# Performance work log

Hardware: AMD Instinct MI355X
Metric: run time of the kernel (lower is better)

The kernel has to match this reference:

```python
import jax, jax.numpy as jnp
import numpy as np
from jax.scipy.special import erfc
from jax.scipy.linalg import solve_triangular

B, N, M = 1024, 256, 320


def _conv(x, w, b, s):
    # torch Conv2d(k=5, stride=s, padding=2)
    y = jax.lax.conv_general_dilated(x, w, (s, s), ((2, 2), (2, 2)),
                                     dimension_numbers=('NCHW', 'OIHW', 'NCHW'))
    return y + b[None, :, None, None]


def _deconv(x, w, b, s):
    # torch ConvTranspose2d(k=5, stride=s, padding=2, output_padding=s-1); w is [Cin,Cout,5,5]
    w2 = jnp.flip(w, (2, 3)).transpose(1, 0, 2, 3)
    pad = (2, 2 + (s - 1))
    y = jax.lax.conv_general_dilated(x, w2, (1, 1), (pad, pad), lhs_dilation=(s, s),
                                     dimension_numbers=('NCHW', 'OIHW', 'NCHW'))
    return y + b[None, :, None, None]


def _gdn(x, beta, gamma, inverse):
    # divisive normalization: norm = 1x1 conv of x^2 with gamma, plus beta
    norm = jnp.einsum('oc,bchw->bohw', gamma, x * x) + beta[None, :, None, None]
    return x * jnp.sqrt(norm) if inverse else x * jax.lax.rsqrt(norm)


def _forward(x, noise, w1, b1, beta1, gamma1, w2, b2, beta2, gamma2, w3, b3,
             dw1, db1, ibeta1, igamma1, dw2, db2, ibeta2, igamma2, dw3, db3,
             mean, scale, H):
    # analysis transform g_a
    a = _gdn(_conv(x, w1, b1, 2), beta1, gamma1, False)   # [B,N,16,16]
    a = _gdn(_conv(a, w2, b2, 2), beta2, gamma2, False)   # [B,N,8,8]
    y = _conv(a, w3, b3, 1)                               # [B,M,8,8]
    Bs, C, h, w = y.shape
    yf = y.reshape(Bs, C, h * w)                          # [B,M,64]
    mask = jnp.tril(jnp.ones((64, 64), jnp.float32), -1)  # strictly lower
    H_tril = H * mask                                     # [M,64,64]
    # w_res = (I - H_tril) y, per channel
    w_res = yf - jnp.einsum('cij,bcj->bci', H_tril, yf)
    # GaussianConditional training-mode quantize: additive uniform noise
    w_res_hat = w_res + noise.reshape(Bs, C, h * w)
    # likelihoods under N(mean, scale) with scale lower bound 0.11
    s = jnp.maximum(scale, 0.11)[None]                    # [1,M,8,8]
    v = jnp.abs(w_res_hat.reshape(Bs, C, h, w) - mean[None])
    c = -(2 ** -0.5)
    upper = 0.5 * erfc(c * ((0.5 - v) / s))
    lower = 0.5 * erfc(c * ((-0.5 - v) / s))
    lik = jnp.maximum(upper - lower, 1e-9)
    # y_hat = (I - H_tril)^{-1} w_res_hat via unit-lower triangular solve
    A = jnp.eye(64, dtype=jnp.float32)[None] - H_tril     # [M,64,64]
    y_hat = solve_triangular(A, w_res_hat.transpose(1, 2, 0), lower=True,
                             unit_diagonal=True).transpose(2, 0, 1).reshape(Bs, C, h, w)
    # synthesis transform g_s
    d = _gdn(_deconv(y_hat, dw1, db1, 1), ibeta1, igamma1, True)
    d = _gdn(_deconv(d, dw2, db2, 2), ibeta2, igamma2, True)
    x_hat = jnp.clip(_deconv(d, dw3, db3, 2), 0.0, 1.0)
    return x_hat, lik


def setup_inputs() -> dict:
    key = jax.random.key(0)
    ks = jax.random.split(key, 16)
    rn = lambda k, sh: 0.02 * jax.random.normal(k, sh, dtype=jnp.float32)
    eye_g = 0.1 * jnp.eye(N, dtype=jnp.float32) + 1e-3
    return {
        'x': jax.random.uniform(ks[0], (B, 2, 32, 32), dtype=jnp.float32),
        'noise': jax.random.uniform(ks[1], (B, M, 8, 8), dtype=jnp.float32) - 0.5,
        'w1': rn(ks[2], (N, 2, 5, 5)), 'b1': jnp.zeros((N,), jnp.float32),
        'beta1': jnp.ones((N,), jnp.float32), 'gamma1': eye_g,
        'w2': rn(ks[3], (N, N, 5, 5)), 'b2': jnp.zeros((N,), jnp.float32),
        'beta2': jnp.ones((N,), jnp.float32), 'gamma2': eye_g,
        'w3': rn(ks[4], (M, N, 5, 5)), 'b3': jnp.zeros((M,), jnp.float32),
        'dw1': rn(ks[5], (M, N, 5, 5)), 'db1': jnp.zeros((N,), jnp.float32),
        'ibeta1': jnp.ones((N,), jnp.float32), 'igamma1': eye_g,
        'dw2': rn(ks[6], (N, N, 5, 5)), 'db2': jnp.zeros((N,), jnp.float32),
        'ibeta2': jnp.ones((N,), jnp.float32), 'igamma2': eye_g,
        'dw3': rn(ks[7], (N, 2, 5, 5)), 'db3': jnp.zeros((2,), jnp.float32),
        'mean': jnp.zeros((M, 8, 8), jnp.float32),
        'scale': jnp.ones((M, 8, 8), jnp.float32),
        'H': rn(ks[8], (M, 64, 64)),
    }


def reference(x, noise, w1, b1, beta1, gamma1, w2, b2, beta2, gamma2, w3, b3,
              dw1, db1, ibeta1, igamma1, dw2, db2, ibeta2, igamma2, dw3, db3,
              mean, scale, H):
    return _forward(x, noise, w1, b1, beta1, gamma1, w2, b2, beta2, gamma2, w3, b3,
                    dw1, db1, ibeta1, igamma1, dw2, db2, ibeta2, igamma2, dw3, db3,
                    mean, scale, H)
```

## Files before the change

### kernel.cpp

```cpp
#include <hip/hip_runtime.h>
#include <math.h>

typedef unsigned short u16;
typedef unsigned long long u64t;
typedef __bf16 bf16x8 __attribute__((ext_vector_type(8)));
typedef float f32x4 __attribute__((ext_vector_type(4)));
struct alignas(8) u16x4 { u16 x0, x1, x2, x3; };

__device__ __forceinline__ int ufl(int v) { return __builtin_amdgcn_readfirstlane(v); }
__device__ __forceinline__ u16 f2b(float f) {
    unsigned u = __float_as_uint(f);
    return (u16)((u + 0x7FFFu + ((u >> 16) & 1u)) >> 16);
}
__device__ __forceinline__ float b2f(u16 h) { return __uint_as_float(((unsigned)h) << 16); }
__device__ __forceinline__ u16 tob(float v) { return f2b(v); }
__device__ __forceinline__ u16 tob(u16 v)   { return v; }


template<int CIN, int COUT>
__global__ __launch_bounds__(256) void rk_fwd(const float* __restrict__ w, u16* __restrict__ a) {
    int j = (blockIdx.x * 256 + threadIdx.x) * 2;
    if (j >= 25 * COUT * CIN) return;
    int ci = j % CIN; int r = j / CIN; int co = r % COUT; int t = r / COUT;
    u16 lo = f2b(w[(co * CIN + ci) * 25 + t]);
    u16 hi = f2b(w[(co * CIN + ci + 1) * 25 + t]);
    *(unsigned*)&a[j] = (unsigned)lo | ((unsigned)hi << 16);
}
__global__ __launch_bounds__(256) void rk_d1(const float* __restrict__ w, u16* __restrict__ a) {
    int j = (blockIdx.x * 256 + threadIdx.x) * 2;
    if (j >= 25 * 256 * 320) return;
    int ci = j % 320; int r = j / 320; int co = r % 256; int tp = r / 256;
    int ky = 4 - tp / 5, kx = 4 - tp % 5;
    u16 lo = f2b(w[(ci * 256 + co) * 25 + ky * 5 + kx]);
    u16 hi = f2b(w[((ci + 1) * 256 + co) * 25 + ky * 5 + kx]);
    *(unsigned*)&a[j] = (unsigned)lo | ((unsigned)hi << 16);
}
__global__ __launch_bounds__(256) void rk_d2(const float* __restrict__ w, u16* __restrict__ a) {
    int j = (blockIdx.x * 256 + threadIdx.x) * 2;
    if (j >= 36 * 256 * 256) return;
    int ci = j % 256; int r = j / 256; int co = r % 256; int qt = r / 256;
    int q = qt / 9, tt = qt % 9;
    int qy = q >> 1, qx = q & 1, ty = tt / 3, tx = tt % 3;
    u16 lo = 0, hi = 0;
    if (ty < 3 - qy && tx < 3 - qx) {
        int widx = (qy + 2 * ty) * 5 + (qx + 2 * tx);
        lo = f2b(w[(ci * 256 + co) * 25 + widx]);
        hi = f2b(w[((ci + 1) * 256 + co) * 25 + widx]);
    }
    *(unsigned*)&a[j] = (unsigned)lo | ((unsigned)hi << 16);
}
__global__ __launch_bounds__(256) void rk_d3(const float* __restrict__ w, float* __restrict__ a) {
    int i = blockIdx.x * 256 + threadIdx.x;
    if (i >= 4 * 256 * 2 * 16) return;
    int t = i % 16; int r = i / 16; int co = r % 2; int r2 = r / 2; int ci = r2 % 256; int q = r2 / 256;
    int qy = q >> 1, qx = q & 1;
    float v = 0.f;
    if (t < 9) {
        int ty = t / 3, tx = t % 3;
        if (ty < 3 - qy && tx < 3 - qx) v = w[(ci * 2 + co) * 25 + (qy + 2 * ty) * 5 + (qx + 2 * tx)];
    }
    a[i] = v;
}
__global__ __launch_bounds__(256) void rk_g(const float* __restrict__ g, u16* __restrict__ a) {
    int j = (blockIdx.x * 256 + threadIdx.x) * 2;
    if (j >= 256 * 256) return;
    u16 lo = f2b(g[j]);
    u16 hi = f2b(g[j + 1]);
    *(unsigned*)&a[j] = (unsigned)lo | ((unsigned)hi << 16);
}

template<int CIN, int COUT, int S, int MT, typename TIN, typename TOUT>
__global__ __launch_bounds__(256)
void mconv(const TIN* __restrict__ in, const u16* __restrict__ A,
           const float* __restrict__ bias, TOUT* __restrict__ out)
{
    constexpr bool O16 = (sizeof(TOUT) == 2);
    constexpr int HIN = 8 * S, HP = 7 * S + 5, CHUNK = 64, STRIDE = CHUNK + 8;
    constexpr int NCH = CIN / CHUNK;
    constexpr int SP = HP * HP;
    constexpr int BSE = SP * STRIDE;
    constexpr int OSE = O16 ? COUT * 64 : 0;
    constexpr int NIT = 50;
    __shared__ u16 bs[(BSE > OSE) ? BSE : OSE];

    const int b = blockIdx.x;
    const int tid = threadIdx.x;
    const int lane = tid & 63, wv = tid >> 6;
    const int lm = lane & 15, quad = lane >> 4;
    const int cob = wv * (MT * 16);
    const TIN* inb = in + (size_t)b * CIN * (HIN * HIN);

    int bofs[4];
#pragma unroll
    for (int nt = 0; nt < 4; ++nt) {
        int px = nt * 16 + lm, oy = px >> 3, ox = px & 7;
        bofs[nt] = (S * oy * HP + S * ox) * STRIDE + quad * 8;
    }

    f32x4 acc[MT][4];
#pragma unroll
    for (int m = 0; m < MT; ++m)
#pragma unroll
        for (int n = 0; n < 4; ++n) acc[m][n] = (f32x4){0.f, 0.f, 0.f, 0.f};

#pragma unroll 1
    for (int ch = 0; ch < NCH; ++ch) {
        if (ch) __syncthreads();
        unsigned* bz = (unsigned*)bs;
        for (int i = tid; i < BSE / 2; i += 256) bz[i] = 0u;
        __syncthreads();
        for (int i = tid; i < (CHUNK / 4) * (HIN * HIN); i += 256) {
            int px = i % (HIN * HIN), cg = i / (HIN * HIN);
            int iy = px / HIN, ix = px % HIN;
            const TIN* ip = inb + (size_t)(ch * CHUNK + cg * 4) * (HIN * HIN) + px;
            u16x4 p;
            p.x0 = tob(ip[0]);
            p.x1 = tob(ip[HIN * HIN]);
            p.x2 = tob(ip[2 * HIN * HIN]);
            p.x3 = tob(ip[3 * HIN * HIN]);
            *(u16x4*)&bs[((iy + 2) * HP + ix + 2) * STRIDE + cg * 4] = p;
        }
        __syncthreads();

        const u16* Ar[MT];
#pragma unroll
        for (int m = 0; m < MT; ++m)
            Ar[m] = A + ch * CHUNK + quad * 8 + (size_t)(cob + m * 16 + lm) * CIN;

        bf16x8 af0[MT], af1[MT];
#pragma unroll
        for (int m = 0; m < MT; ++m) af0[m] = *(const bf16x8*)(Ar[m]);

#pragma unroll 1
        for (int it = 0; it < NIT; it += 2) {
            const int tapB = (it + 1) >> 1, kcB = (it + 1) & 1;
            const size_t oB = (size_t)tapB * (COUT * CIN) + kcB * 32;
#pragma unroll
            for (int m = 0; m < MT; ++m) af1[m] = *(const bf16x8*)(Ar[m] + oB);
            {
                const int tap = it >> 1, kc = it & 1;
                const int tofs = ((tap / 5) * HP + (tap % 5)) * STRIDE + kc * 32;
                bf16x8 bf[4];
#pragma unroll
                for (int nt = 0; nt < 4; ++nt)
                    bf[nt] = *(const bf16x8*)&bs[bofs[nt] + tofs];
#pragma unroll
                for (int m = 0; m < MT; ++m)
#pragma unroll
                    for (int nt = 0; nt < 4; ++nt)
                        acc[m][nt] = __builtin_amdgcn_mfma_f32_16x16x32_bf16(af0[m], bf[nt], acc[m][nt], 0, 0, 0);
            }
            if (it + 2 < NIT) {
                const size_t oC = (size_t)((it + 2) >> 1) * (COUT * CIN);
#pragma unroll
                for (int m = 0; m < MT; ++m) af0[m] = *(const bf16x8*)(Ar[m] + oC);
            }
            {
                const int tofs = ((tapB / 5) * HP + (tapB % 5)) * STRIDE + kcB * 32;
                bf16x8 bf[4];
#pragma unroll
                for (int nt = 0; nt < 4; ++nt)
                    bf[nt] = *(const bf16x8*)&bs[bofs[nt] + tofs];
#pragma unroll
                for (int m = 0; m < MT; ++m)
#pragma unroll
                    for (int nt = 0; nt < 4; ++nt)
                        acc[m][nt] = __builtin_amdgcn_mfma_f32_16x16x32_bf16(af1[m], bf[nt], acc[m][nt], 0, 0, 0);
            }
        }
    }

    if constexpr (O16) {
        __syncthreads();
#pragma unroll
        for (int m = 0; m < MT; ++m)
#pragma unroll
            for (int nt = 0; nt < 4; ++nt)
#pragma unroll
                for (int r = 0; r < 4; ++r) {
                    int co = cob + m * 16 + quad * 4 + r;
                    bs[co * 64 + nt * 16 + lm] = f2b(acc[m][nt][r] + bias[co]);
                }
        __syncthreads();
        u16* ob = out + (size_t)b * COUT * 64;
        const unsigned* osw = (const unsigned*)bs;
#pragma unroll
        for (int it = 0; it < COUT / 16; ++it) {
            int v = it * 256 + tid;
            unsigned lo = osw[v * 2], hi = osw[v * 2 + 1];
            *(u64t*)&ob[v * 4] = (u64t)lo | ((u64t)hi << 32);
        }
    } else {
        float* ob = (float*)out + (size_t)b * COUT * 64;
#pragma unroll
        for (int m = 0; m < MT; ++m)
#pragma unroll
            for (int nt = 0; nt < 4; ++nt) {
                int px = nt * 16 + lm;
#pragma unroll
                for (int r = 0; r < 4; ++r) {
                    int co = cob + m * 16 + quad * 4 + r;
                    ob[(size_t)co * 64 + px] = acc[m][nt][r] + bias[co];
                }
            }
    }
}

template<bool INVERSE, int IMG, int YOFF, int RS>
__global__ __launch_bounds__(256)
void gdnm(u16* __restrict__ x, const float* __restrict__ beta,
          const u16* __restrict__ Ag)
{
    constexpr int STR = 264;
    __shared__ u16 xb[256 * 64];
    __shared__ u16 xq[64 * STR];
    const int tid = threadIdx.x;
    const int lane = tid & 63, wv = tid >> 6;
    const int lm = lane & 15, quad = lane >> 4;
    const int cob = wv * 64;
    u16* xg = x + (size_t)blockIdx.x * IMG + (size_t)blockIdx.y * YOFF;

#pragma unroll
    for (int it = 0; it < 16; ++it) {
        int v = it * 256 + tid;
        int ch = v >> 4, pxg = (v & 15) * 4;
        *(u64t*)&xb[v * 4] = *(const u64t*)&xg[(size_t)ch * RS + pxg];
    }
    __syncthreads();

    {
        const int px = tid & 63, g = tid >> 6;
#pragma unroll
        for (int w = 0; w < 32; ++w) {
            int ci = g * 64 + ((w + px) & 31) * 2;
            float x0 = b2f(xb[ci * 64 + px]);
            float x1 = b2f(xb[(ci + 1) * 64 + px]);
            unsigned pk = (unsigned)f2b(x0 * x0) | ((unsigned)f2b(x1 * x1) << 16);
            *(unsigned*)&xq[px * STR + ci] = pk;
        }
    }
    __syncthreads();

    f32x4 acc[4][4];
#pragma unroll
    for (int m = 0; m < 4; ++m)
#pragma unroll
        for (int n = 0; n < 4; ++n) acc[m][n] = (f32x4){0.f, 0.f, 0.f, 0.f};

#pragma unroll 1
    for (int kc = 0; kc < 8; ++kc) {
        bf16x8 bf[4];
#pragma unroll
        for (int nt = 0; nt < 4; ++nt)
            bf[nt] = *(const bf16x8*)&xq[(nt * 16 + lm) * STR + kc * 32 + quad * 8];
        bf16x8 af[4];
#pragma unroll
        for (int m = 0; m < 4; ++m)
            af[m] = *(const bf16x8*)(Ag + (size_t)(cob + m * 16 + lm) * 256 + kc * 32 + quad * 8);
#pragma unroll
        for (int m = 0; m < 4; ++m)
#pragma unroll
            for (int nt = 0; nt < 4; ++nt)
                acc[m][nt] = __builtin_amdgcn_mfma_f32_16x16x32_bf16(af[m], bf[nt], acc[m][nt], 0, 0, 0);
    }

#pragma unroll
    for (int m = 0; m < 4; ++m)
#pragma unroll
        for (int nt = 0; nt < 4; ++nt)
#pragma unroll
            for (int r = 0; r < 4; ++r) {
                int co = cob + m * 16 + quad * 4 + r;
                int px = nt * 16 + lm;
                float norm = acc[m][nt][r] + beta[co];
                float rr = INVERSE ? sqrtf(norm) : rsqrtf(norm);
                u16* p = &xb[co * 64 + px];
                *p = f2b(b2f(*p) * rr);
            }
    __syncthreads();

#pragma unroll
    for (int it = 0; it < 16; ++it) {
        int v = it * 256 + tid;
        int ch = v >> 4, pxg = (v & 15) * 4;
        *(u64t*)&xg[(size_t)ch * RS + pxg] = *(const u64t*)&xb[v * 4];
    }
}

__global__ __launch_bounds__(256)
void mdeconv2(const u16* __restrict__ in, const u16* __restrict__ A2,
              const float* __restrict__ bias, u16* __restrict__ out)
{
    constexpr int STRIDE = 264;
    __shared__ u16 bs[100 * STRIDE];
    __shared__ u16 os[256 * 64];
    const int b = blockIdx.x, tid = threadIdx.x;
    const int lane = tid & 63, wv = tid >> 6, lm = lane & 15, quad = lane >> 4;
    const int cob = wv * 64;
    const u16* inb = in + (size_t)b * 256 * 64;

    unsigned* bz = (unsigned*)bs;
    for (int i = tid; i < 100 * STRIDE / 2; i += 256) bz[i] = 0u;
    __syncthreads();
    for (int i = tid; i < 64 * 64; i += 256) {
        int px = i & 63, cg = i >> 6;
        int iy = px >> 3, ix = px & 7;
        const u16* ip = inb + (size_t)cg * 4 * 64 + px;
        u16x4 p;
        p.x0 = ip[0]; p.x1 = ip[64]; p.x2 = ip[128]; p.x3 = ip[192];
        *(u16x4*)&bs[((iy + 1) * 10 + ix + 1) * STRIDE + cg * 4] = p;
    }
    __syncthreads();

    int bofs[4];
#pragma unroll
    for (int nt = 0; nt < 4; ++nt) {
        int sp = nt * 16 + lm, sy = sp >> 3, sx = sp & 7;
        bofs[nt] = ((sy + 2) * 10 + sx + 2) * STRIDE + quad * 8;
    }

#pragma unroll
    for (int qy = 0; qy < 2; ++qy)
#pragma unroll
        for (int qx = 0; qx < 2; ++qx) {
            const int q = qy * 2 + qx;
            const int W = 3 - qx;
            const int NT = (3 - qy) * W;
            const int NITq = NT * 8;
            f32x4 acc[4][4];
#pragma unroll
            for (int m = 0; m < 4; ++m)
#pragma unroll
                for (int n = 0; n < 4; ++n) acc[m][n] = (f32x4){0.f, 0.f, 0.f, 0.f};

            const u16* Ar[4];
#pragma unroll
            for (int m = 0; m < 4; ++m)
                Ar[m] = A2 + (size_t)(q * 9) * 65536 + quad * 8 + (size_t)(cob + m * 16 + lm) * 256;

            bf16x8 af0[4], af1[4];
#pragma unroll
            for (int m = 0; m < 4; ++m) af0[m] = *(const bf16x8*)(Ar[m]);

#pragma unroll 1
            for (int it = 0; it < NITq; it += 2) {
                const int itB = it + 1;
                const int ttB = itB >> 3, kcB = itB & 7;
                const int tyB = ttB / W, txB = ttB % W;
                const size_t oB = (size_t)(tyB * 3 + txB) * 65536 + kcB * 32;
#pragma unroll
                for (int m = 0; m < 4; ++m) af1[m] = *(const bf16x8*)(Ar[m] + oB);
                {
                    const int tt = it >> 3, kc = it & 7;
                    const int ty = tt / W, tx = tt % W;
                    const int boff = -(ty * 10 + tx) * STRIDE + kc * 32;
                    bf16x8 bf[4];
#pragma unroll
                    for (int nt = 0; nt < 4; ++nt)
                        bf[nt] = *(const bf16x8*)&bs[bofs[nt] + boff];
#pragma unroll
                    for (int m = 0; m < 4; ++m)
#pragma unroll
                        for (int nt = 0; nt < 4; ++nt)
                            acc[m][nt] = __builtin_amdgcn_mfma_f32_16x16x32_bf16(af0[m], bf[nt], acc[m][nt], 0, 0, 0);
                }
                if (it + 2 < NITq) {
                    const int ttC = (it + 2) >> 3, kcC = (it + 2) & 7;
                    const int tyC = ttC / W, txC = ttC % W;
                    const size_t oC = (size_t)(tyC * 3 + txC) * 65536 + kcC * 32;
#pragma unroll
                    for (int m = 0; m < 4; ++m) af0[m] = *(const bf16x8*)(Ar[m] + oC);
                }
                {
                    const int boff = -(tyB * 10 + txB) * STRIDE + kcB * 32;
                    bf16x8 bf[4];
#pragma unroll
                    for (int nt = 0; nt < 4; ++nt)
                        bf[nt] = *(const bf16x8*)&bs[bofs[nt] + boff];
#pragma unroll
                    for (int m = 0; m < 4; ++m)
#pragma unroll
                        for (int nt = 0; nt < 4; ++nt)
                            acc[m][nt] = __builtin_amdgcn_mfma_f32_16x16x32_bf16(af1[m], bf[nt], acc[m][nt], 0, 0, 0);
                }
            }
#pragma unroll
            for (int m = 0; m < 4; ++m)
#pragma unroll
                for (int nt = 0; nt < 4; ++nt)
#pragma unroll
                    for (int r = 0; r < 4; ++r) {
                        int co = cob + m * 16 + quad * 4 + r;
                        os[co * 64 + nt * 16 + lm] = f2b(acc[m][nt][r] + bias[co]);
                    }
            __syncthreads();
            u16* od = out + ((size_t)(b * 4 + q)) * 256 * 64;
            const unsigned* osw = (const unsigned*)os;
#pragma unroll
            for (int it = 0; it < 16; ++it) {
                int v = it * 256 + tid;
                unsigned lo = osw[v * 2], hi = osw[v * 2 + 1];
                *(u64t*)&od[v * 4] = (u64t)lo | ((u64t)hi << 32);
            }
            __syncthreads();
        }
}

__global__ __launch_bounds__(256)
void dec3k(const u16* __restrict__ in, const float* __restrict__ W3r,
           const float* __restrict__ bias, float* __restrict__ out)
{
    constexpr int HT = 18;
    __shared__ float ls[32 * HT * HT];
    const int b = blockIdx.x, tid = threadIdx.x;
    const int sy = tid >> 4, sx = tid & 15;
    const u16* inb = in + (size_t)b * 4 * 256 * 64;
    float acc[4][2] = {};
#pragma unroll 1
    for (int ch = 0; ch < 8; ++ch) {
        if (ch) __syncthreads();
        for (int i = tid; i < 32 * HT * HT; i += 256) ls[i] = 0.f;
        __syncthreads();
        for (int i = tid; i < 32 * 256; i += 256) {
            int ci = i >> 8, px = i & 255, iy = px >> 4, ix = px & 15;
            int q = (iy & 1) * 2 + (ix & 1);
            int sp = (iy >> 1) * 8 + (ix >> 1);
            ls[ci * (HT * HT) + (iy + 1) * HT + ix + 1] =
                b2f(inb[((size_t)q * 256 + ch * 32 + ci) * 64 + sp]);
        }
        __syncthreads();
#pragma unroll 1
        for (int ci = 0; ci < 32; ++ci) {
            float v[9];
            const float* l = &ls[ci * (HT * HT) + (sy + 2) * HT + sx + 2];
#pragma unroll
            for (int ty = 0; ty < 3; ++ty)
#pragma unroll
                for (int tx = 0; tx < 3; ++tx) v[ty * 3 + tx] = l[-(ty * HT) - tx];
#pragma unroll
            for (int q = 0; q < 4; ++q) {
                const float* wp = W3r + (size_t)ufl(((q * 256 + ch * 32 + ci) * 2) * 16);
#pragma unroll
                for (int t = 0; t < 9; ++t) {
                    acc[q][0] = fmaf(wp[t], v[t], acc[q][0]);
                    acc[q][1] = fmaf(wp[16 + t], v[t], acc[q][1]);
                }
            }
        }
    }
    float* ob = out + (size_t)b * 2 * 1024;
#pragma unroll
    for (int q = 0; q < 4; ++q) {
        int qy = q >> 1, qx = q & 1;
        int oy = 2 * sy + qy, ox = 2 * sx + qx;
#pragma unroll
        for (int co = 0; co < 2; ++co) {
            float r = acc[q][co] + bias[co];
            r = fminf(fmaxf(r, 0.f), 1.f);
            ob[(size_t)co * 1024 + oy * 32 + ox] = r;
        }
    }
}

template<int CIN, int COUT, int HIN, int WIN, int S, int CI_CHUNK, int CO_PER_BLOCK>
__global__ __launch_bounds__(256)
void conv5k(const float* __restrict__ in, const float* __restrict__ wt,
            const float* __restrict__ bias, u16* __restrict__ out)
{
    constexpr int HOUT = HIN / S, WOUT = WIN / S;
    constexpr int PX = HOUT * WOUT;
    constexpr int CO_ITERS = CO_PER_BLOCK;
    constexpr int HT = HIN + 4, WT = WIN + 4;
    constexpr int NCHUNK = CIN / CI_CHUNK;
    constexpr int TILE = CI_CHUNK * HT * WT;

    __shared__ float lds[TILE];
    __shared__ u16 os[CO_PER_BLOCK * PX];

    const int b = blockIdx.x;
    const int co_base = blockIdx.y * CO_PER_BLOCK;
    const int tid = threadIdx.x;
    const int px = tid;
    const int oy = px / WOUT, ox = px % WOUT;

    float acc[CO_ITERS];
#pragma unroll
    for (int i = 0; i < CO_ITERS; ++i) acc[i] = 0.f;

    const float* inb = in + (size_t)b * CIN * HIN * WIN;

#pragma unroll 1
    for (int ch = 0; ch < NCHUNK; ++ch) {
        if (ch) __syncthreads();
        for (int idx = tid; idx < TILE; idx += 256) lds[idx] = 0.f;
        __syncthreads();
        for (int idx = tid; idx < CI_CHUNK * HIN * WIN; idx += 256) {
            int ci = idx / (HIN * WIN);
            int r = idx - ci * (HIN * WIN);
            int iy = r / WIN, ix = r - iy * WIN;
            lds[ci * (HT * WT) + (iy + 2) * WT + (ix + 2)] =
                inb[(size_t)(ch * CI_CHUNK + ci) * (HIN * WIN) + r];
        }
        __syncthreads();

#pragma unroll 1
        for (int ci = 0; ci < CI_CHUNK; ++ci) {
            float v[25];
            const float* l = &lds[ci * (HT * WT) + (oy * S) * WT + (ox * S)];
#pragma unroll
            for (int ky = 0; ky < 5; ++ky)
#pragma unroll
                for (int kx = 0; kx < 5; ++kx)
                    v[ky * 5 + kx] = l[ky * WT + kx];
#pragma unroll
            for (int i = 0; i < CO_ITERS; ++i) {
                const int co = co_base + i;
                const float* wp = wt + (size_t)ufl((co * CIN + ch * CI_CHUNK + ci) * 25);
#pragma unroll
                for (int t = 0; t < 25; ++t) acc[i] = fmaf(wp[t], v[t], acc[i]);
            }
        }
    }

#pragma unroll
    for (int i = 0; i < CO_ITERS; ++i)
        os[i * PX + px] = f2b(acc[i] + bias[co_base + i]);
    __syncthreads();
    u16* ob = out + ((size_t)b * COUT + co_base) * PX;
    const unsigned* osw = (const unsigned*)os;
#pragma unroll
    for (int it = 0; it < CO_PER_BLOCK * PX / 1024; ++it) {
        int v = it * 256 + tid;
        unsigned lo = osw[v * 2], hi = osw[v * 2 + 1];
        *(u64t*)&ob[v * 4] = (u64t)lo | ((u64t)hi << 32);
    }
}

__global__ __launch_bounds__(256)
void trik(float* __restrict__ y, const float* __restrict__ noise,
          const float* __restrict__ H, const float* __restrict__ mean,
          const float* __restrict__ scale, float* __restrict__ lik)
{
    __shared__ float h[64 * 65];
    const int c = blockIdx.x;
    const int bt = blockIdx.y;
    const int tid = threadIdx.x;
    const int lane = tid & 63;
    const int wv = tid >> 6;

    const float* Hc = H + (size_t)c * 4096;
    for (int idx = tid; idx < 4096; idx += 256) {
        const int i = idx >> 6, j = idx & 63;
        h[i * 65 + j] = Hc[idx];
    }
    __syncthreads();

    const int b = bt * 4 + wv;
    const size_t base = ((size_t)b * 320 + c) * 64 + lane;
    const float* hrow = &h[lane * 65];

    const float yv = y[base];
    float ws = 0.f;
#pragma unroll 8
    for (int j = 0; j < 64; ++j) {
        const float yj = __shfl(yv, j, 64);
        const float hv = (j < lane) ? hrow[j] : 0.f;
        ws = fmaf(hv, yj, ws);
    }
    const float wh = yv - ws + noise[base];

    const float mn = mean[c * 64 + lane];
    const float sc = fmaxf(scale[c * 64 + lane], 0.11f);
    const float vv = fabsf(wh - mn);
    const float cst = -0.70710678118654752f;
    const float upper = 0.5f * erfcf(cst * (0.5f - vv) / sc);
    const float lower = 0.5f * erfcf(cst * (-0.5f - vv) / sc);
    lik[base] = fmaxf(upper - lower, 1e-9f);

    float acc = wh;
#pragma unroll 8
    for (int j = 0; j < 64; ++j) {
        const float yj = __shfl(acc, j, 64);
        const float hv = (j < lane) ? hrow[j] : 0.f;
        acc = fmaf(hv, yj, acc);
    }
    y[base] = acc;
}

extern "C" void kernel_launch(void* const* d_in, const int* in_sizes, int n_in,
                              void* d_out, int out_size, void* d_ws, size_t ws_size,
                              hipStream_t stream)
{
    (void)in_sizes; (void)n_in; (void)out_size; (void)ws_size;

    const float* x      = (const float*)d_in[0];
    const float* noise  = (const float*)d_in[1];
    const float* w1     = (const float*)d_in[2];
    const float* b1     = (const float*)d_in[3];
    const float* beta1  = (const float*)d_in[4];
    const float* gamma1 = (const float*)d_in[5];
    const float* w2     = (const float*)d_in[6];
    const float* b2     = (const float*)d_in[7];
    const float* beta2  = (const float*)d_in[8];
    const float* gamma2 = (const float*)d_in[9];
    const float* w3     = (const float*)d_in[10];
    const float* b3     = (const float*)d_in[11];
    const float* dw1    = (const float*)d_in[12];
    const float* db1    = (const float*)d_in[13];
    const float* ibeta1 = (const float*)d_in[14];
    const float* igamma1= (const float*)d_in[15];
    const float* dw2    = (const float*)d_in[16];
    const float* db2    = (const float*)d_in[17];
    const float* ibeta2 = (const float*)d_in[18];
    const float* igamma2= (const float*)d_in[19];
    const float* dw3    = (const float*)d_in[20];
    const float* db3    = (const float*)d_in[21];
    const float* mean   = (const float*)d_in[22];
    const float* scale  = (const float*)d_in[23];
    const float* H      = (const float*)d_in[24];

    float* outp = (float*)d_out;
    float* xhat = outp;
    float* lik  = outp + (size_t)1024 * 2 * 32 * 32;

    char* ws = (char*)d_ws;
    u16*   a1  = (u16*)ws;
    float* y   = (float*)ws;
    u16*   d2  = (u16*)ws;
    u16*   a2  = (u16*)(ws + 134217728);
    u16*   d1  = (u16*)(ws + 134217728);
    u16*   Ag1 = (u16*)(ws + 167772160);
    u16*   Ag2 = (u16*)(ws + 167903232);
    u16*   Ag3 = (u16*)(ws + 168034304);
    u16*   Ag4 = (u16*)(ws + 168165376);
    u16*   Ac2 = (u16*)(ws + 201326592);
    u16*   Ac3 = (u16*)(ws + 204603392);
    u16*   Ad1 = (u16*)(ws + 208699392);
    u16*   Ad2 = (u16*)(ws + 212795392);
    float* W3r = (float*)(ws + 217513984);

    rk_fwd<256, 256><<<3200, 256, 0, stream>>>(w2, Ac2);
    rk_fwd<256, 320><<<4000, 256, 0, stream>>>(w3, Ac3);
    rk_d1<<<4000, 256, 0, stream>>>(dw1, Ad1);
    rk_d2<<<4608, 256, 0, stream>>>(dw2, Ad2);
    rk_d3<<<128, 256, 0, stream>>>(dw3, W3r);
    rk_g<<<128, 256, 0, stream>>>(gamma1, Ag1);
    rk_g<<<128, 256, 0, stream>>>(gamma2, Ag2);
    rk_g<<<128, 256, 0, stream>>>(igamma1, Ag3);
    rk_g<<<128, 256, 0, stream>>>(igamma2, Ag4);

    conv5k<2, 256, 32, 32, 2, 2, 16><<<dim3(1024, 16), 256, 0, stream>>>(x, w1, b1, a1);
    gdnm<false, 65536, 64, 256><<<dim3(1024, 4), 256, 0, stream>>>(a1, beta1, Ag1);
    mconv<256, 256, 2, 4, u16, u16><<<1024, 256, 0, stream>>>(a1, Ac2, b2, a2);
    gdnm<false, 16384, 16384, 64><<<dim3(1024, 1), 256, 0, stream>>>(a2, beta2, Ag2);
    mconv<256, 320, 1, 5, u16, float><<<1024, 256, 0, stream>>>(a2, Ac3, b3, y);

    trik<<<dim3(320, 256), 256, 0, stream>>>(y, noise, H, mean, scale, lik);

    mconv<320, 256, 1, 4, float, u16><<<1024, 256, 0, stream>>>(y, Ad1, db1, d1);
    gdnm<true, 16384, 16384, 64><<<dim3(1024, 1), 256, 0, stream>>>(d1, ibeta1, Ag3);
    mdeconv2<<<1024, 256, 0, stream>>>(d1, Ad2, db2, d2);
    gdnm<true, 65536, 16384, 64><<<dim3(1024, 4), 256, 0, stream>>>(d2, ibeta2, Ag4);
    dec3k<<<1024, 256, 0, stream>>>(d2, W3r, db3, xhat);
}
```

Before: 3.466 ms.

## Replace shuffle-based triangular solve with precomputed inverse and bf16 MFMA matmuls

Each call now precomputes a masked bf16 copy of H and the strictly-lower part of the inverse of (I - H_tril) per channel. The shuffle-serial forward substitution becomes two batched 64x64 matrix products on MFMA over 64-sample tiles. The aim is to drop the per-wave serial dependency chain and the many small blocks, in exchange for bf16 rounding of y and w_hat in the matmuls. It also adds a serial inversion kernel to setup.

```diff
diff --git a/kernel.cpp b/kernel.cpp
--- a/kernel.cpp
+++ b/kernel.cpp
@@ -67,6 +67,51 @@
     u16 lo = f2b(g[j]);
     u16 hi = f2b(g[j + 1]);
     *(unsigned*)&a[j] = (unsigned)lo | ((unsigned)hi << 16);
+}
+__global__ __launch_bounds__(256) void rk_hb(const float* __restrict__ H, u16* __restrict__ a) {
+    int p = blockIdx.x * 256 + threadIdx.x;
+    if (p >= 320 * 2048) return;
+    int j2 = (p & 31) * 2;
+    int r = p >> 5;
+    int i = r & 63;
+    u16 lo = (j2 < i) ? f2b(H[(size_t)r * 64 + j2]) : (u16)0;
+    u16 hi = (j2 + 1 < i) ? f2b(H[(size_t)r * 64 + j2 + 1]) : (u16)0;
+    *(unsigned*)&a[(size_t)r * 64 + j2] = (unsigned)lo | ((unsigned)hi << 16);
+}
+__global__ __launch_bounds__(256)
+void rk_inv(const float* __restrict__ H, u16* __restrict__ Mb)
+{
+    __shared__ float Ls[64 * 68];
+    __shared__ float Ms[64 * 68];
+    const int c = blockIdx.x, tid = threadIdx.x;
+    const float* Hc = H + (size_t)c * 4096;
+#pragma unroll
+    for (int it = 0; it < 16; ++it) {
+        int v = it * 256 + tid;
+        int i = v >> 6, j = v & 63;
+        Ls[i * 68 + j] = (j < i) ? Hc[v] : 0.f;
+    }
+    __syncthreads();
+    if (tid < 64) {
+        const int j = tid;
+#pragma unroll 1
+        for (int i = 0; i < 64; ++i) {
+            float s = (i == j) ? 1.f : 0.f;
+#pragma unroll 1
+            for (int k = 0; k < i; ++k)
+                s = fmaf(Ls[i * 68 + k], Ms[k * 68 + j], s);
+            Ms[i * 68 + j] = s;
+        }
+    }
+    __syncthreads();
+#pragma unroll
+    for (int it = 0; it < 8; ++it) {
+        int p = it * 256 + tid;
+        int i = p >> 5, j2 = (p & 31) * 2;
+        u16 lo = (j2 < i) ? f2b(Ms[i * 68 + j2]) : (u16)0;
+        u16 hi = (j2 + 1 < i) ? f2b(Ms[i * 68 + j2 + 1]) : (u16)0;
+        *(unsigned*)&Mb[(size_t)c * 4096 + i * 64 + j2] = (unsigned)lo | ((unsigned)hi << 16);
+    }
 }
 
 template<int CIN, int COUT, int S, int MT, typename TIN, typename TOUT>
@@ -537,54 +582,96 @@
 }
 
 __global__ __launch_bounds__(256)
-void trik(float* __restrict__ y, const float* __restrict__ noise,
-          const float* __restrict__ H, const float* __restrict__ mean,
-          const float* __restrict__ scale, float* __restrict__ lik)
+void trik_m(float* __restrict__ y, const float* __restrict__ noise,
+            const u16* __restrict__ Hb, const u16* __restrict__ Mb,
+            const float* __restrict__ mean, const float* __restrict__ scale,
+            float* __restrict__ lik)
 {
-    __shared__ float h[64 * 65];
+    __shared__ float Ysf[64 * 68];
+    __shared__ u16 Yt[64 * 72];
     const int c = blockIdx.x;
-    const int bt = blockIdx.y;
+    const int b0 = blockIdx.y * 64;
     const int tid = threadIdx.x;
-    const int lane = tid & 63;
-    const int wv = tid >> 6;
-
-    const float* Hc = H + (size_t)c * 4096;
-    for (int idx = tid; idx < 4096; idx += 256) {
-        const int i = idx >> 6, j = idx & 63;
-        h[i * 65 + j] = Hc[idx];
-    }
-    __syncthreads();
-
-    const int b = bt * 4 + wv;
-    const size_t base = ((size_t)b * 320 + c) * 64 + lane;
-    const float* hrow = &h[lane * 65];
-
-    const float yv = y[base];
-    float ws = 0.f;
-#pragma unroll 8
-    for (int j = 0; j < 64; ++j) {
-        const float yj = __shfl(yv, j, 64);
-        const float hv = (j < lane) ? hrow[j] : 0.f;
-        ws = fmaf(hv, yj, ws);
-    }
-    const float wh = yv - ws + noise[base];
-
-    const float mn = mean[c * 64 + lane];
-    const float sc = fmaxf(scale[c * 64 + lane], 0.11f);
-    const float vv = fabsf(wh - mn);
-    const float cst = -0.70710678118654752f;
-    const float upper = 0.5f * erfcf(cst * (0.5f - vv) / sc);
-    const float lower = 0.5f * erfcf(cst * (-0.5f - vv) / sc);
-    lik[base] = fmaxf(upper - lower, 1e-9f);
-
-    float acc = wh;
-#pragma unroll 8
-    for (int j = 0; j < 64; ++j) {
-        const float yj = __shfl(acc, j, 64);
-        const float hv = (j < lane) ? hrow[j] : 0.f;
-        acc = fmaf(hv, yj, acc);
-    }
-    y[base] = acc;
+    const int lane = tid & 63, wv = tid >> 6;
+    const int lm = lane & 15, quad = lane >> 4;
+    const int cob = wv * 16;
+
+#pragma unroll
+    for (int it = 0; it < 4; ++it) {
+        int v = it * 256 + tid;
+        int b = v >> 4, i0 = (v & 15) * 4;
+        f32x4 t = *(const f32x4*)(y + (size_t)(b0 + b) * 20480 + c * 64 + i0);
+        *(f32x4*)&Ysf[b * 68 + i0] = t;
+        u16x4 p;
+        p.x0 = f2b(t[0]); p.x1 = f2b(t[1]); p.x2 = f2b(t[2]); p.x3 = f2b(t[3]);
+        *(u16x4*)&Yt[b * 72 + i0] = p;
+    }
+    __syncthreads();
+
+    f32x4 acc[4];
+#pragma unroll
+    for (int nt = 0; nt < 4; ++nt) acc[nt] = (f32x4){0.f, 0.f, 0.f, 0.f};
+    const u16* Ha = Hb + (size_t)c * 4096 + (cob + lm) * 64 + quad * 8;
+#pragma unroll
+    for (int kc = 0; kc < 2; ++kc) {
+        bf16x8 af = *(const bf16x8*)(Ha + kc * 32);
+#pragma unroll
+        for (int nt = 0; nt < 4; ++nt) {
+            bf16x8 bf = *(const bf16x8*)&Yt[(nt * 16 + lm) * 72 + kc * 32 + quad * 8];
+            acc[nt] = __builtin_amdgcn_mfma_f32_16x16x32_bf16(af, bf, acc[nt], 0, 0, 0);
+        }
+    }
+    __syncthreads();
+
+    const int i0 = cob + quad * 4;
+    const f32x4 mn4 = *(const f32x4*)(mean + c * 64 + i0);
+    const f32x4 sc4 = *(const f32x4*)(scale + c * 64 + i0);
+    float whf[4][4];
+#pragma unroll
+    for (int nt = 0; nt < 4; ++nt) {
+        int b = nt * 16 + lm;
+        f32x4 nz = *(const f32x4*)(noise + (size_t)(b0 + b) * 20480 + c * 64 + i0);
+        f32x4 lk;
+#pragma unroll
+        for (int r = 0; r < 4; ++r) {
+            float wh = Ysf[b * 68 + i0 + r] - acc[nt][r] + nz[r];
+            whf[nt][r] = wh;
+            const float sc = fmaxf(sc4[r], 0.11f);
+            const float vv = fabsf(wh - mn4[r]);
+            const float cst = -0.70710678118654752f;
+            const float upper = 0.5f * erfcf(cst * (0.5f - vv) / sc);
+            const float lower = 0.5f * erfcf(cst * (-0.5f - vv) / sc);
+            lk[r] = fmaxf(upper - lower, 1e-9f);
+        }
+        *(f32x4*)(lik + (size_t)(b0 + b) * 20480 + c * 64 + i0) = lk;
+        u16x4 p;
+        p.x0 = f2b(whf[nt][0]); p.x1 = f2b(whf[nt][1]);
+        p.x2 = f2b(whf[nt][2]); p.x3 = f2b(whf[nt][3]);
+        *(u16x4*)&Yt[b * 72 + i0] = p;
+    }
+    __syncthreads();
+
+    f32x4 acc2[4];
+#pragma unroll
+    for (int nt = 0; nt < 4; ++nt) acc2[nt] = (f32x4){0.f, 0.f, 0.f, 0.f};
+    const u16* Ma = Mb + (size_t)c * 4096 + (cob + lm) * 64 + quad * 8;
+#pragma unroll
+    for (int kc = 0; kc < 2; ++kc) {
+        bf16x8 af = *(const bf16x8*)(Ma + kc * 32);
+#pragma unroll
+        for (int nt = 0; nt < 4; ++nt) {
+            bf16x8 bf = *(const bf16x8*)&Yt[(nt * 16 + lm) * 72 + kc * 32 + quad * 8];
+            acc2[nt] = __builtin_amdgcn_mfma_f32_16x16x32_bf16(af, bf, acc2[nt], 0, 0, 0);
+        }
+    }
+#pragma unroll
+    for (int nt = 0; nt < 4; ++nt) {
+        int b = nt * 16 + lm;
+        f32x4 yh;
+#pragma unroll
+        for (int r = 0; r < 4; ++r) yh[r] = whf[nt][r] + acc2[nt][r];
+        *(f32x4*)(y + (size_t)(b0 + b) * 20480 + c * 64 + i0) = yh;
+    }
 }
 
 extern "C" void kernel_launch(void* const* d_in, const int* in_sizes, int n_in,
@@ -633,6 +720,8 @@
     u16*   Ag2 = (u16*)(ws + 167903232);
     u16*   Ag3 = (u16*)(ws + 168034304);
     u16*   Ag4 = (u16*)(ws + 168165376);
+    u16*   Hb  = (u16*)(ws + 168296448);
+    u16*   Mb  = (u16*)(ws + 170917888);
     u16*   Ac2 = (u16*)(ws + 201326592);
     u16*   Ac3 = (u16*)(ws + 204603392);
     u16*   Ad1 = (u16*)(ws + 208699392);
@@ -648,6 +737,8 @@
     rk_g<<<128, 256, 0, stream>>>(gamma2, Ag2);
     rk_g<<<128, 256, 0, stream>>>(igamma1, Ag3);
     rk_g<<<128, 256, 0, stream>>>(igamma2, Ag4);
+    rk_hb<<<2560, 256, 0, stream>>>(H, Hb);
+    rk_inv<<<320, 256, 0, stream>>>(H, Mb);
 
     conv5k<2, 256, 32, 32, 2, 2, 16><<<dim3(1024, 16), 256, 0, stream>>>(x, w1, b1, a1);
     gdnm<false, 65536, 64, 256><<<dim3(1024, 4), 256, 0, stream>>>(a1, beta1, Ag1);
@@ -655,7 +746,7 @@
     gdnm<false, 16384, 16384, 64><<<dim3(1024, 1), 256, 0, stream>>>(a2, beta2, Ag2);
     mconv<256, 320, 1, 5, u16, float><<<1024, 256, 0, stream>>>(a2, Ac3, b3, y);
 
-    trik<<<dim3(320, 256), 256, 0, stream>>>(y, noise, H, mean, scale, lik);
+    trik_m<<<dim3(320, 16), 256, 0, stream>>>(y, noise, Hb, Mb, mean, scale, lik);
 
     mconv<320, 256, 1, 4, float, u16><<<1024, 256, 0, stream>>>(y, Ad1, db1, d1);
     gdnm<true, 16384, 16384, 64><<<dim3(1024, 1), 256, 0, stream>>>(d1, ibeta1, Ag3);
```

Result: faster. 3.036 ms (-12.4%).
